# Kernel tuning notes

Hardware: AMD Instinct MI355X
Metric: run time of the kernel (lower is better)

## Reference

```python
import jax, jax.numpy as jnp
import numpy as np

D_MODEL = 256
NHEAD = 8
HEAD_DIM = D_MODEL // NHEAD
CLIP = 10.0


def setup_inputs() -> dict:
    key = jax.random.key(0)
    k1, k2, k3, k4 = jax.random.split(key, 4)
    B, N = 4, 256
    nodes = jax.random.normal(k1, (B, N, D_MODEL), dtype=jnp.float32)
    edges = jax.random.normal(k2, (B, N, N, D_MODEL), dtype=jnp.float32)
    # torch nn.Linear default init: U(-1/sqrt(in), 1/sqrt(in))
    bound = 1.0 / np.sqrt(D_MODEL)
    W = jax.random.uniform(k3, (D_MODEL, D_MODEL), minval=-bound, maxval=bound, dtype=jnp.float32)
    b = jax.random.uniform(k4, (D_MODEL,), minval=-bound, maxval=bound, dtype=jnp.float32)
    return {"nodes": nodes, "edges": edges, "W": W, "b": b}


def reference(nodes, edges, W, b):
    B, N, _ = nodes.shape
    H, Dh = NHEAD, HEAD_DIM

    def proj(x):  # torch Linear: x @ W.T + b
        return x @ W.T + b

    # Node projections: the module applies the SAME linear to q, k, v
    node_p = proj(nodes).reshape(B, N, H, Dh)
    nq, nk, nv = node_p, node_p, node_p
    # Edge projections (same linear for q and k)
    edge_p = proj(edges).reshape(B, N, N, H, Dh)
    eq, ek = edge_p, edge_p

    query = eq + nq[:, :, None, :, :]   # (B,N,N,H,Dh)
    key = ek + nk[:, None, :, :, :]     # (B,N,N,H,Dh)
    scores = jnp.einsum('bijhd,bijhd->bhij', query, key) / np.sqrt(Dh).astype(np.float32)
    scores = CLIP * jnp.tanh(scores)
    attn = jax.nn.softmax(scores, axis=-1)  # (B,H,N,N)
    # output = attn @ values (values transposed to (B,H,N,Dh))
    out = jnp.einsum('bhij,bjhd->bihd', attn, nv).reshape(B, N, D_MODEL)
    out = proj(out)
    return (out, attn)
```

## Files before the change

### kernel.cpp

```cpp
#include <hip/hip_runtime.h>
#include <hip/hip_bf16.h>
#include <math.h>

typedef short short8 __attribute__((ext_vector_type(8)));
typedef float f32x4 __attribute__((ext_vector_type(4)));

__device__ __forceinline__ unsigned short f2bf(float x) {
    unsigned u = __float_as_uint(x);
    u += 0x7FFF + ((u >> 16) & 1);
    return (unsigned short)(u >> 16);
}
__device__ __forceinline__ float bf2f(unsigned short h) {
    return __uint_as_float(((unsigned)h) << 16);
}

__device__ __forceinline__ void cvtpair(float f0, float f1, unsigned& hw, unsigned& lw) {
    __hip_bfloat162 h2 = __float22bfloat162_rn(float2{f0, f1});
    unsigned hu = *(unsigned*)&h2;
    float r0 = f0 - __uint_as_float(hu << 16);
    float r1 = f1 - __uint_as_float(hu & 0xFFFF0000u);
    __hip_bfloat162 l2 = __float22bfloat162_rn(float2{r0, r1});
    hw = hu;
    lw = *(unsigned*)&l2;
}

__device__ __forceinline__ void cvt8(const float4 a, const float4 b, short8& hi, short8& lo) {
    union { unsigned u[4]; short8 s; } H, L;
    cvtpair(a.x, a.y, H.u[0], L.u[0]);
    cvtpair(a.z, a.w, H.u[1], L.u[1]);
    cvtpair(b.x, b.y, H.u[2], L.u[2]);
    cvtpair(b.z, b.w, H.u[3], L.u[3]);
    hi = H.s; lo = L.s;
}

__device__ __forceinline__ float tanh10(float y) {
    float e = __expf(2.f * y);
    return 10.f * (e - 1.f) / (e + 1.f);
}

#define GLDS16(gp, lp)                                                        \
    __builtin_amdgcn_global_load_lds(                                         \
        (const __attribute__((address_space(1))) void*)(gp),                  \
        (__attribute__((address_space(3))) void*)(lp), 16, 0, 0)

__global__ __launch_bounds__(256) void k_prep(const float* __restrict__ W,
                                              float* __restrict__ Wt,
                                              unsigned short* __restrict__ Whi,
                                              unsigned short* __restrict__ Wlo) {
    int d = blockIdx.x, k = threadIdx.x;
    float w = W[d * 256 + k];
    Wt[k * 256 + d] = w;
    unsigned short hi = f2bf(w);
    int s  = (k >> 3) & 3;
    int sp = s ^ ((d >> 1) & 3);
    int idx = d * 256 + (k & ~31) + sp * 8 + (k & 7);
    Whi[idx] = hi;
    Wlo[idx] = f2bf(w - bf2f(hi));
}

__global__ __launch_bounds__(256) void k_node_proj(const float* __restrict__ nodes,
                                                   const float* __restrict__ Wt,
                                                   const float* __restrict__ bias,
                                                   float* __restrict__ np_) {
    int row = blockIdx.x;
    int d = threadIdx.x;
    __shared__ float xl[256];
    xl[d] = nodes[row * 256 + d];
    __syncthreads();
    float a[8] = {0.f, 0.f, 0.f, 0.f, 0.f, 0.f, 0.f, 0.f};
#pragma unroll 4
    for (int k = 0; k < 256; k += 8) {
#pragma unroll
        for (int q = 0; q < 8; ++q)
            a[q] = fmaf(xl[k + q], Wt[(k + q) * 256 + d], a[q]);
    }
    np_[row * 256 + d] =
        bias[d] + ((a[0] + a[1]) + (a[2] + a[3])) + ((a[4] + a[5]) + (a[6] + a[7]));
}

__global__ __launch_bounds__(256, 2) void k_edge_mfma(const float* __restrict__ edges,
                                                      const unsigned short* __restrict__ Whi,
                                                      const unsigned short* __restrict__ Wlo,
                                                      const float* __restrict__ bias,
                                                      const float* __restrict__ np_,
                                                      float* __restrict__ attn) {
    __shared__ unsigned short Wbuf[2][2][128 * 32];
    __shared__ float npi[128];
    __shared__ float sc[4][256];

    const int t = threadIdx.x;
    const int w = t >> 6, l = t & 63;
    const int col = l & 15, g = l >> 4;
    const int wrow = l >> 2, wq = l & 3;

    const int p = blockIdx.x;
    const int L = (p & 7) * 256 + (p >> 3);
    const int tile = L >> 1, half = L & 1;
    const int bb = tile >> 8, ii = tile & 255;
    const int n0 = half * 128;

    if (t < 32)
        ((float4*)npi)[t] = ((const float4*)(np_ + (size_t)(bb * 256 + ii) * 256 + n0))[t];
    __builtin_amdgcn_sched_barrier(0);

    f32x4 acc[4][8];
#pragma unroll
    for (int mt = 0; mt < 4; ++mt)
#pragma unroll
        for (int nt = 0; nt < 8; ++nt) acc[mt][nt] = (f32x4){0.f, 0.f, 0.f, 0.f};

    const float* ea = edges + ((size_t)((bb * 256 + ii) * 256 + w * 64 + col)) * 256 + g * 8;
    const size_t wg0 = (size_t)(n0 + w * 32 + wrow) * 256 + wq * 8;
    const size_t wg1 = wg0 + 16 * 256;

    GLDS16(Whi + wg0, &Wbuf[0][0][(w * 32) * 32]);
    GLDS16(Wlo + wg0, &Wbuf[0][1][(w * 32) * 32]);
    GLDS16(Whi + wg1, &Wbuf[0][0][(w * 32 + 16) * 32]);
    GLDS16(Wlo + wg1, &Wbuf[0][1][(w * 32 + 16) * 32]);
    __builtin_amdgcn_sched_barrier(0);
    float4 e[4][2];
#pragma unroll
    for (int mt = 0; mt < 4; ++mt) {
        e[mt][0] = *(const float4*)(ea + mt * 4096);
        e[mt][1] = *(const float4*)(ea + mt * 4096 + 4);
    }
    __builtin_amdgcn_sched_barrier(0);
    asm volatile("s_waitcnt vmcnt(8)\n\ts_barrier" ::: "memory");

    const int swb = (g ^ ((col >> 1) & 3)) << 3;

    short8 Ah[4], Al[4];

#pragma unroll
    for (int kc = 0; kc < 8; ++kc) {
#pragma unroll
        for (int mt = 0; mt < 4; ++mt)
            cvt8(e[mt][0], e[mt][1], Ah[mt], Al[mt]);
        __builtin_amdgcn_sched_barrier(0);
        if (kc < 7) {
            const int nb = (kc + 1) & 1;
            const size_t kofs = (size_t)(kc + 1) * 32;
            GLDS16(Whi + wg0 + kofs, &Wbuf[nb][0][(w * 32) * 32]);
            GLDS16(Wlo + wg0 + kofs, &Wbuf[nb][1][(w * 32) * 32]);
            GLDS16(Whi + wg1 + kofs, &Wbuf[nb][0][(w * 32 + 16) * 32]);
            GLDS16(Wlo + wg1 + kofs, &Wbuf[nb][1][(w * 32 + 16) * 32]);
            __builtin_amdgcn_sched_barrier(0);
#pragma unroll
            for (int mt = 0; mt < 4; ++mt) {
                e[mt][0] = *(const float4*)(ea + (kc + 1) * 32 + mt * 4096);
                e[mt][1] = *(const float4*)(ea + (kc + 1) * 32 + mt * 4096 + 4);
            }
            __builtin_amdgcn_sched_barrier(0);
        }
        const unsigned short* bh = &Wbuf[kc & 1][0][0] + col * 32 + swb;
        const unsigned short* bl = &Wbuf[kc & 1][1][0] + col * 32 + swb;
        __builtin_amdgcn_s_setprio(1);
#pragma unroll
        for (int nt = 0; nt < 8; ++nt) {
            short8 Bh = *(const short8*)(bh + nt * 512);
            short8 Bl = *(const short8*)(bl + nt * 512);
#pragma unroll
            for (int mt = 0; mt < 4; ++mt) {
                acc[mt][nt] = __builtin_amdgcn_mfma_f32_16x16x32_bf16(Ah[mt], Bh, acc[mt][nt], 0, 0, 0);
                acc[mt][nt] = __builtin_amdgcn_mfma_f32_16x16x32_bf16(Ah[mt], Bl, acc[mt][nt], 0, 0, 0);
                acc[mt][nt] = __builtin_amdgcn_mfma_f32_16x16x32_bf16(Al[mt], Bh, acc[mt][nt], 0, 0, 0);
            }
        }
        __builtin_amdgcn_s_setprio(0);
        __builtin_amdgcn_sched_barrier(0);
        if (kc < 7) {
            asm volatile("s_waitcnt vmcnt(8)\n\ts_barrier" ::: "memory");
        }
    }

    const float isq = 0.17677669529663687f;
    float bv[8], nv[8];
#pragma unroll
    for (int nt = 0; nt < 8; ++nt) {
        int dl = nt * 16 + col;
        bv[nt] = bias[n0 + dl];
        nv[nt] = npi[dl];
    }
#pragma unroll
    for (int mt = 0; mt < 4; ++mt) {
#pragma unroll
        for (int r = 0; r < 4; ++r) {
            int el = w * 64 + mt * 16 + g * 4 + r;
            const float* npj = np_ + (size_t)(bb * 256 + el) * 256 + n0;
            float pp, s0 = 0.f, s1 = 0.f, s2 = 0.f, s3 = 0.f;
            pp = acc[mt][0][r] + bv[0]; s0 += (pp + nv[0]) * (pp + npj[col]);
            pp = acc[mt][1][r] + bv[1]; s0 += (pp + nv[1]) * (pp + npj[16 + col]);
            pp = acc[mt][2][r] + bv[2]; s1 += (pp + nv[2]) * (pp + npj[32 + col]);
            pp = acc[mt][3][r] + bv[3]; s1 += (pp + nv[3]) * (pp + npj[48 + col]);
            pp = acc[mt][4][r] + bv[4]; s2 += (pp + nv[4]) * (pp + npj[64 + col]);
            pp = acc[mt][5][r] + bv[5]; s2 += (pp + nv[5]) * (pp + npj[80 + col]);
            pp = acc[mt][6][r] + bv[6]; s3 += (pp + nv[6]) * (pp + npj[96 + col]);
            pp = acc[mt][7][r] + bv[7]; s3 += (pp + nv[7]) * (pp + npj[112 + col]);
#pragma unroll
            for (int m = 1; m < 16; m <<= 1) {
                s0 += __shfl_xor(s0, m, 64);
                s1 += __shfl_xor(s1, m, 64);
                s2 += __shfl_xor(s2, m, 64);
                s3 += __shfl_xor(s3, m, 64);
            }
            if (col == 0) {
                sc[0][el] = tanh10(s0 * isq);
                sc[1][el] = tanh10(s1 * isq);
                sc[2][el] = tanh10(s2 * isq);
                sc[3][el] = tanh10(s3 * isq);
            }
        }
    }
    __syncthreads();

    {
        float4 v = *(float4*)&sc[w][l * 4];
        float m = fmaxf(fmaxf(v.x, v.y), fmaxf(v.z, v.w));
#pragma unroll
        for (int s = 1; s < 64; s <<= 1) m = fmaxf(m, __shfl_xor(m, s, 64));
        v.x = __expf(v.x - m); v.y = __expf(v.y - m);
        v.z = __expf(v.z - m); v.w = __expf(v.w - m);
        float sum = v.x + v.y + v.z + v.w;
#pragma unroll
        for (int s = 1; s < 64; s <<= 1) sum += __shfl_xor(sum, s, 64);
        float inv = 1.f / sum;
        v.x *= inv; v.y *= inv; v.z *= inv; v.w *= inv;
        *(float4*)(attn + (((size_t)(bb * 8 + half * 4 + w) * 256 + ii) << 8) + l * 4) = v;
    }
}

__global__ __launch_bounds__(256) void k_out(const float* __restrict__ attn,
                                             const float* __restrict__ np_,
                                             const float* __restrict__ Wt,
                                             const float* __restrict__ bias,
                                             float* __restrict__ out) {
    int bi = blockIdx.x;
    int bb = bi >> 8, ii = bi & 255;
    int d = threadIdx.x;
    __shared__ float at[8 * 256];
    __shared__ float xl[256];
#pragma unroll
    for (int s = 0; s < 2; ++s) {
        int idx = d + s * 256;
        int h = idx >> 6, q = idx & 63;
        ((float4*)at)[idx] =
            ((const float4*)(attn + ((size_t)(bb * 8 + h) * 256 + ii) * 256))[q];
    }
    __syncthreads();
    int h = d >> 5;
    const float* npb = np_ + (size_t)bb * 65536 + d;
    const float* ath = at + h * 256;
    float a[8] = {0.f, 0.f, 0.f, 0.f, 0.f, 0.f, 0.f, 0.f};
#pragma unroll 2
    for (int j = 0; j < 256; j += 8) {
#pragma unroll
        for (int q = 0; q < 8; ++q)
            a[q] = fmaf(ath[j + q], npb[(size_t)(j + q) * 256], a[q]);
    }
    xl[d] = ((a[0] + a[1]) + (a[2] + a[3])) + ((a[4] + a[5]) + (a[6] + a[7]));
    __syncthreads();
    float c[8] = {bias[d], 0.f, 0.f, 0.f, 0.f, 0.f, 0.f, 0.f};
#pragma unroll 2
    for (int k = 0; k < 256; k += 8) {
#pragma unroll
        for (int q = 0; q < 8; ++q)
            c[q] = fmaf(xl[k + q], Wt[(k + q) * 256 + d], c[q]);
    }
    out[bi * 256 + d] =
        ((c[0] + c[1]) + (c[2] + c[3])) + ((c[4] + c[5]) + (c[6] + c[7]));
}

extern "C" void kernel_launch(void* const* d_in, const int* in_sizes, int n_in,
                              void* d_out, int out_size, void* d_ws, size_t ws_size,
                              hipStream_t stream) {
    (void)in_sizes; (void)n_in; (void)out_size; (void)ws_size;
    const float* nodes = (const float*)d_in[0];
    const float* edges = (const float*)d_in[1];
    const float* W     = (const float*)d_in[2];
    const float* bias  = (const float*)d_in[3];

    float* out  = (float*)d_out;
    float* attn = out + 262144;

    float* np_ = (float*)d_ws;
    float* Wt  = np_ + 262144;
    unsigned short* Whi = (unsigned short*)(Wt + 65536);
    unsigned short* Wlo = Whi + 65536;

    hipLaunchKernelGGL(k_prep,      dim3(256),  dim3(256), 0, stream, W, Wt, Whi, Wlo);
    hipLaunchKernelGGL(k_node_proj, dim3(1024), dim3(256), 0, stream, nodes, Wt, bias, np_);
    hipLaunchKernelGGL(k_edge_mfma, dim3(2048), dim3(256), 0, stream, edges, Whi, Wlo, bias, np_, attn);
    hipLaunchKernelGGL(k_out,       dim3(1024), dim3(256), 0, stream, attn, np_, Wt, bias, out);
}
```

Before: 478.1 us.

## Split edge projection into column quarters with fully preloaded W slice in LDS

```diff
diff --git a/kernel.cpp b/kernel.cpp
--- a/kernel.cpp
+++ b/kernel.cpp
@@ -51,9 +51,9 @@
     float w = W[d * 256 + k];
     Wt[k * 256 + d] = w;
     unsigned short hi = f2bf(w);
-    int s  = (k >> 3) & 3;
-    int sp = s ^ ((d >> 1) & 3);
-    int idx = d * 256 + (k & ~31) + sp * 8 + (k & 7);
+    int G  = k >> 3;
+    int Gp = G ^ (d & 7);
+    int idx = d * 256 + Gp * 8 + (k & 7);
     Whi[idx] = hi;
     Wlo[idx] = f2bf(w - bf2f(hi));
 }
@@ -84,81 +84,92 @@
                                                       const float* __restrict__ bias,
                                                       const float* __restrict__ np_,
                                                       float* __restrict__ attn) {
-    __shared__ unsigned short Wbuf[2][2][128 * 32];
-    __shared__ float npi[128];
-    __shared__ float sc[4][256];
+    __shared__ unsigned short Wf[2][64 * 256];
+    __shared__ float npi[64];
+    __shared__ float sc[2][256];
 
     const int t = threadIdx.x;
     const int w = t >> 6, l = t & 63;
     const int col = l & 15, g = l >> 4;
-    const int wrow = l >> 2, wq = l & 3;
+    const int cx = col & 7;
 
     const int p = blockIdx.x;
-    const int L = (p & 7) * 256 + (p >> 3);
-    const int tile = L >> 1, half = L & 1;
+    const int L = (p & 7) * 512 + (p >> 3);
+    const int tile = L >> 2, quarter = L & 3;
     const int bb = tile >> 8, ii = tile & 255;
-    const int n0 = half * 128;
-
-    if (t < 32)
-        ((float4*)npi)[t] = ((const float4*)(np_ + (size_t)(bb * 256 + ii) * 256 + n0))[t];
+    const int n0 = quarter * 64;
+
+    float4 npiv = ((const float4*)(np_ + (size_t)(bb * 256 + ii) * 256 + n0))[l & 15];
     __builtin_amdgcn_sched_barrier(0);
 
-    f32x4 acc[4][8];
+#pragma unroll
+    for (int m = 0; m < 2; ++m) {
+        const unsigned short* gs = (m ? Wlo : Whi) +
+            (size_t)(n0 + w * 16 + (l >> 5)) * 256 + (l & 31) * 8;
+#pragma unroll
+        for (int i = 0; i < 8; ++i)
+            GLDS16(gs + (size_t)(2 * i) * 256, &Wf[m][(w * 16 + 2 * i) * 256]);
+    }
+    __builtin_amdgcn_sched_barrier(0);
+
+    const float* ea = edges + ((size_t)((bb * 256 + ii) * 256 + w * 64 + col)) * 256 + g * 8;
+    float4 e0[4][2], e1[4][2];
+#pragma unroll
+    for (int mt = 0; mt < 4; ++mt) {
+        e0[mt][0] = *(const float4*)(ea + mt * 4096);
+        e0[mt][1] = *(const float4*)(ea + mt * 4096 + 4);
+    }
+#pragma unroll
+    for (int mt = 0; mt < 4; ++mt) {
+        e1[mt][0] = *(const float4*)(ea + 32 + mt * 4096);
+        e1[mt][1] = *(const float4*)(ea + 32 + mt * 4096 + 4);
+    }
+    if (l < 16) ((float4*)npi)[l] = npiv;
+    __builtin_amdgcn_sched_barrier(0);
+    asm volatile("s_waitcnt vmcnt(16) lgkmcnt(0)\n\ts_barrier" ::: "memory");
+
+    f32x4 acc[4][4];
 #pragma unroll
     for (int mt = 0; mt < 4; ++mt)
 #pragma unroll
-        for (int nt = 0; nt < 8; ++nt) acc[mt][nt] = (f32x4){0.f, 0.f, 0.f, 0.f};
-
-    const float* ea = edges + ((size_t)((bb * 256 + ii) * 256 + w * 64 + col)) * 256 + g * 8;
-    const size_t wg0 = (size_t)(n0 + w * 32 + wrow) * 256 + wq * 8;
-    const size_t wg1 = wg0 + 16 * 256;
-
-    GLDS16(Whi + wg0, &Wbuf[0][0][(w * 32) * 32]);
-    GLDS16(Wlo + wg0, &Wbuf[0][1][(w * 32) * 32]);
-    GLDS16(Whi + wg1, &Wbuf[0][0][(w * 32 + 16) * 32]);
-    GLDS16(Wlo + wg1, &Wbuf[0][1][(w * 32 + 16) * 32]);
-    __builtin_amdgcn_sched_barrier(0);
-    float4 e[4][2];
-#pragma unroll
-    for (int mt = 0; mt < 4; ++mt) {
-        e[mt][0] = *(const float4*)(ea + mt * 4096);
-        e[mt][1] = *(const float4*)(ea + mt * 4096 + 4);
-    }
-    __builtin_amdgcn_sched_barrier(0);
-    asm volatile("s_waitcnt vmcnt(8)\n\ts_barrier" ::: "memory");
-
-    const int swb = (g ^ ((col >> 1) & 3)) << 3;
+        for (int nt = 0; nt < 4; ++nt) acc[mt][nt] = (f32x4){0.f, 0.f, 0.f, 0.f};
 
     short8 Ah[4], Al[4];
 
 #pragma unroll
     for (int kc = 0; kc < 8; ++kc) {
-#pragma unroll
-        for (int mt = 0; mt < 4; ++mt)
-            cvt8(e[mt][0], e[mt][1], Ah[mt], Al[mt]);
+        if (kc & 1) {
+#pragma unroll
+            for (int mt = 0; mt < 4; ++mt) cvt8(e1[mt][0], e1[mt][1], Ah[mt], Al[mt]);
+        } else {
+#pragma unroll
+            for (int mt = 0; mt < 4; ++mt) cvt8(e0[mt][0], e0[mt][1], Ah[mt], Al[mt]);
+        }
         __builtin_amdgcn_sched_barrier(0);
-        if (kc < 7) {
-            const int nb = (kc + 1) & 1;
-            const size_t kofs = (size_t)(kc + 1) * 32;
-            GLDS16(Whi + wg0 + kofs, &Wbuf[nb][0][(w * 32) * 32]);
-            GLDS16(Wlo + wg0 + kofs, &Wbuf[nb][1][(w * 32) * 32]);
-            GLDS16(Whi + wg1 + kofs, &Wbuf[nb][0][(w * 32 + 16) * 32]);
-            GLDS16(Wlo + wg1 + kofs, &Wbuf[nb][1][(w * 32 + 16) * 32]);
-            __builtin_amdgcn_sched_barrier(0);
-#pragma unroll
-            for (int mt = 0; mt < 4; ++mt) {
-                e[mt][0] = *(const float4*)(ea + (kc + 1) * 32 + mt * 4096);
-                e[mt][1] = *(const float4*)(ea + (kc + 1) * 32 + mt * 4096 + 4);
-            }
-            __builtin_amdgcn_sched_barrier(0);
-        }
-        const unsigned short* bh = &Wbuf[kc & 1][0][0] + col * 32 + swb;
-        const unsigned short* bl = &Wbuf[kc & 1][1][0] + col * 32 + swb;
+        if (kc < 6) {
+            if (kc & 1) {
+#pragma unroll
+                for (int mt = 0; mt < 4; ++mt) {
+                    e1[mt][0] = *(const float4*)(ea + (kc + 2) * 32 + mt * 4096);
+                    e1[mt][1] = *(const float4*)(ea + (kc + 2) * 32 + mt * 4096 + 4);
+                }
+            } else {
+#pragma unroll
+                for (int mt = 0; mt < 4; ++mt) {
+                    e0[mt][0] = *(const float4*)(ea + (kc + 2) * 32 + mt * 4096);
+                    e0[mt][1] = *(const float4*)(ea + (kc + 2) * 32 + mt * 4096 + 4);
+                }
+            }
+        }
+        __builtin_amdgcn_sched_barrier(0);
+        const int gofs = (((kc << 2) | g) ^ cx) << 3;
+        const unsigned short* bh = &Wf[0][col * 256 + gofs];
+        const unsigned short* bl = &Wf[1][col * 256 + gofs];
         __builtin_amdgcn_s_setprio(1);
 #pragma unroll
-        for (int nt = 0; nt < 8; ++nt) {
-            short8 Bh = *(const short8*)(bh + nt * 512);
-            short8 Bl = *(const short8*)(bl + nt * 512);
+        for (int nt = 0; nt < 4; ++nt) {
+            short8 Bh = *(const short8*)(bh + nt * 4096);
+            short8 Bl = *(const short8*)(bl + nt * 4096);
 #pragma unroll
             for (int mt = 0; mt < 4; ++mt) {
                 acc[mt][nt] = __builtin_amdgcn_mfma_f32_16x16x32_bf16(Ah[mt], Bh, acc[mt][nt], 0, 0, 0);
@@ -168,15 +179,12 @@
         }
         __builtin_amdgcn_s_setprio(0);
         __builtin_amdgcn_sched_barrier(0);
-        if (kc < 7) {
-            asm volatile("s_waitcnt vmcnt(8)\n\ts_barrier" ::: "memory");
-        }
     }
 
     const float isq = 0.17677669529663687f;
-    float bv[8], nv[8];
-#pragma unroll
-    for (int nt = 0; nt < 8; ++nt) {
+    float bv[4], nv[4];
+#pragma unroll
+    for (int nt = 0; nt < 4; ++nt) {
         int dl = nt * 16 + col;
         bv[nt] = bias[n0 + dl];
         nv[nt] = npi[dl];
@@ -187,33 +195,25 @@
         for (int r = 0; r < 4; ++r) {
             int el = w * 64 + mt * 16 + g * 4 + r;
             const float* npj = np_ + (size_t)(bb * 256 + el) * 256 + n0;
-            float pp, s0 = 0.f, s1 = 0.f, s2 = 0.f, s3 = 0.f;
+            float pp, s0 = 0.f, s1 = 0.f;
             pp = acc[mt][0][r] + bv[0]; s0 += (pp + nv[0]) * (pp + npj[col]);
             pp = acc[mt][1][r] + bv[1]; s0 += (pp + nv[1]) * (pp + npj[16 + col]);
             pp = acc[mt][2][r] + bv[2]; s1 += (pp + nv[2]) * (pp + npj[32 + col]);
             pp = acc[mt][3][r] + bv[3]; s1 += (pp + nv[3]) * (pp + npj[48 + col]);
-            pp = acc[mt][4][r] + bv[4]; s2 += (pp + nv[4]) * (pp + npj[64 + col]);
-            pp = acc[mt][5][r] + bv[5]; s2 += (pp + nv[5]) * (pp + npj[80 + col]);
-            pp = acc[mt][6][r] + bv[6]; s3 += (pp + nv[6]) * (pp + npj[96 + col]);
-            pp = acc[mt][7][r] + bv[7]; s3 += (pp + nv[7]) * (pp + npj[112 + col]);
 #pragma unroll
             for (int m = 1; m < 16; m <<= 1) {
                 s0 += __shfl_xor(s0, m, 64);
                 s1 += __shfl_xor(s1, m, 64);
-                s2 += __shfl_xor(s2, m, 64);
-                s3 += __shfl_xor(s3, m, 64);
             }
             if (col == 0) {
                 sc[0][el] = tanh10(s0 * isq);
                 sc[1][el] = tanh10(s1 * isq);
-                sc[2][el] = tanh10(s2 * isq);
-                sc[3][el] = tanh10(s3 * isq);
-            }
-        }
-    }
-    __syncthreads();
-
-    {
+            }
+        }
+    }
+    __syncthreads();
+
+    if (w < 2) {
         float4 v = *(float4*)&sc[w][l * 4];
         float m = fmaxf(fmaxf(v.x, v.y), fmaxf(v.z, v.w));
 #pragma unroll
@@ -225,7 +225,7 @@
         for (int s = 1; s < 64; s <<= 1) sum += __shfl_xor(sum, s, 64);
         float inv = 1.f / sum;
         v.x *= inv; v.y *= inv; v.z *= inv; v.w *= inv;
-        *(float4*)(attn + (((size_t)(bb * 8 + half * 4 + w) * 256 + ii) << 8) + l * 4) = v;
+        *(float4*)(attn + (((size_t)(bb * 8 + quarter * 2 + w) * 256 + ii) << 8) + l * 4) = v;
     }
 }
 
@@ -289,6 +289,6 @@
 
     hipLaunchKernelGGL(k_prep,      dim3(256),  dim3(256), 0, stream, W, Wt, Whi, Wlo);
     hipLaunchKernelGGL(k_node_proj, dim3(1024), dim3(256), 0, stream, nodes, Wt, bias, np_);
-    hipLaunchKernelGGL(k_edge_mfma, dim3(2048), dim3(256), 0, stream, edges, Whi, Wlo, bias, np_, attn);
+    hipLaunchKernelGGL(k_edge_mfma, dim3(4096), dim3(256), 0, stream, edges, Whi, Wlo, bias, np_, attn);
     hipLaunchKernelGGL(k_out,       dim3(1024), dim3(256), 0, stream, attn, np_, Wt, bias, out);
 }
```

Measured after the change: 524.9 us. 9.8% more time.

## Split edge MFMA block across eight waves with fewer M tiles per wave

Applied to the files above, without the earlier changes.

```diff
diff --git a/kernel.cpp b/kernel.cpp
--- a/kernel.cpp
+++ b/kernel.cpp
@@ -42,6 +42,8 @@
     __builtin_amdgcn_global_load_lds(                                         \
         (const __attribute__((address_space(1))) void*)(gp),                  \
         (__attribute__((address_space(3))) void*)(lp), 16, 0, 0)
+
+#define SB0() __builtin_amdgcn_sched_barrier(0)
 
 __global__ __launch_bounds__(256) void k_prep(const float* __restrict__ W,
                                               float* __restrict__ Wt,
@@ -78,7 +80,7 @@
         bias[d] + ((a[0] + a[1]) + (a[2] + a[3])) + ((a[4] + a[5]) + (a[6] + a[7]));
 }
 
-__global__ __launch_bounds__(256, 2) void k_edge_mfma(const float* __restrict__ edges,
+__global__ __launch_bounds__(512, 4) void k_edge_mfma(const float* __restrict__ edges,
                                                       const unsigned short* __restrict__ Whi,
                                                       const unsigned short* __restrict__ Wlo,
                                                       const float* __restrict__ bias,
@@ -91,7 +93,6 @@
     const int t = threadIdx.x;
     const int w = t >> 6, l = t & 63;
     const int col = l & 15, g = l >> 4;
-    const int wrow = l >> 2, wq = l & 3;
 
     const int p = blockIdx.x;
     const int L = (p & 7) * 256 + (p >> 3);
@@ -101,56 +102,51 @@
 
     if (t < 32)
         ((float4*)npi)[t] = ((const float4*)(np_ + (size_t)(bb * 256 + ii) * 256 + n0))[t];
-    __builtin_amdgcn_sched_barrier(0);
-
-    f32x4 acc[4][8];
-#pragma unroll
-    for (int mt = 0; mt < 4; ++mt)
+    SB0();
+
+    f32x4 acc[2][8];
+#pragma unroll
+    for (int mt = 0; mt < 2; ++mt)
 #pragma unroll
         for (int nt = 0; nt < 8; ++nt) acc[mt][nt] = (f32x4){0.f, 0.f, 0.f, 0.f};
 
-    const float* ea = edges + ((size_t)((bb * 256 + ii) * 256 + w * 64 + col)) * 256 + g * 8;
-    const size_t wg0 = (size_t)(n0 + w * 32 + wrow) * 256 + wq * 8;
-    const size_t wg1 = wg0 + 16 * 256;
-
-    GLDS16(Whi + wg0, &Wbuf[0][0][(w * 32) * 32]);
-    GLDS16(Wlo + wg0, &Wbuf[0][1][(w * 32) * 32]);
-    GLDS16(Whi + wg1, &Wbuf[0][0][(w * 32 + 16) * 32]);
-    GLDS16(Wlo + wg1, &Wbuf[0][1][(w * 32 + 16) * 32]);
-    __builtin_amdgcn_sched_barrier(0);
-    float4 e[4][2];
-#pragma unroll
-    for (int mt = 0; mt < 4; ++mt) {
-        e[mt][0] = *(const float4*)(ea + mt * 4096);
-        e[mt][1] = *(const float4*)(ea + mt * 4096 + 4);
-    }
-    __builtin_amdgcn_sched_barrier(0);
-    asm volatile("s_waitcnt vmcnt(8)\n\ts_barrier" ::: "memory");
+    const float* ea = edges + ((size_t)((bb * 256 + ii) * 256 + w * 32 + col)) * 256 + g * 8;
+    const size_t wg = (size_t)(n0 + w * 16 + (l >> 2)) * 256 + (l & 3) * 8;
+
+    GLDS16(Whi + wg, &Wbuf[0][0][(w * 16) * 32]);
+    GLDS16(Wlo + wg, &Wbuf[0][1][(w * 16) * 32]);
+    SB0();
+    float4 e[2][2];
+    e[0][0] = *(const float4*)(ea);
+    e[0][1] = *(const float4*)(ea + 4);
+    e[1][0] = *(const float4*)(ea + 4096);
+    e[1][1] = *(const float4*)(ea + 4096 + 4);
+    SB0();
+    asm volatile("s_waitcnt vmcnt(4)\n\ts_barrier" ::: "memory");
 
     const int swb = (g ^ ((col >> 1) & 3)) << 3;
 
-    short8 Ah[4], Al[4];
+    short8 Ah[2], Al[2];
 
 #pragma unroll
     for (int kc = 0; kc < 8; ++kc) {
-#pragma unroll
-        for (int mt = 0; mt < 4; ++mt)
-            cvt8(e[mt][0], e[mt][1], Ah[mt], Al[mt]);
-        __builtin_amdgcn_sched_barrier(0);
+        cvt8(e[0][0], e[0][1], Ah[0], Al[0]);
+        SB0();
         if (kc < 7) {
             const int nb = (kc + 1) & 1;
             const size_t kofs = (size_t)(kc + 1) * 32;
-            GLDS16(Whi + wg0 + kofs, &Wbuf[nb][0][(w * 32) * 32]);
-            GLDS16(Wlo + wg0 + kofs, &Wbuf[nb][1][(w * 32) * 32]);
-            GLDS16(Whi + wg1 + kofs, &Wbuf[nb][0][(w * 32 + 16) * 32]);
-            GLDS16(Wlo + wg1 + kofs, &Wbuf[nb][1][(w * 32 + 16) * 32]);
-            __builtin_amdgcn_sched_barrier(0);
-#pragma unroll
-            for (int mt = 0; mt < 4; ++mt) {
-                e[mt][0] = *(const float4*)(ea + (kc + 1) * 32 + mt * 4096);
-                e[mt][1] = *(const float4*)(ea + (kc + 1) * 32 + mt * 4096 + 4);
-            }
-            __builtin_amdgcn_sched_barrier(0);
+            GLDS16(Whi + wg + kofs, &Wbuf[nb][0][(w * 16) * 32]);
+            GLDS16(Wlo + wg + kofs, &Wbuf[nb][1][(w * 16) * 32]);
+            e[0][0] = *(const float4*)(ea + (kc + 1) * 32);
+            e[0][1] = *(const float4*)(ea + (kc + 1) * 32 + 4);
+            SB0();
+        }
+        cvt8(e[1][0], e[1][1], Ah[1], Al[1]);
+        SB0();
+        if (kc < 7) {
+            e[1][0] = *(const float4*)(ea + (kc + 1) * 32 + 4096);
+            e[1][1] = *(const float4*)(ea + (kc + 1) * 32 + 4096 + 4);
+            SB0();
         }
         const unsigned short* bh = &Wbuf[kc & 1][0][0] + col * 32 + swb;
         const unsigned short* bl = &Wbuf[kc & 1][1][0] + col * 32 + swb;
@@ -159,17 +155,17 @@
         for (int nt = 0; nt < 8; ++nt) {
             short8 Bh = *(const short8*)(bh + nt * 512);
             short8 Bl = *(const short8*)(bl + nt * 512);
-#pragma unroll
-            for (int mt = 0; mt < 4; ++mt) {
-                acc[mt][nt] = __builtin_amdgcn_mfma_f32_16x16x32_bf16(Ah[mt], Bh, acc[mt][nt], 0, 0, 0);
-                acc[mt][nt] = __builtin_amdgcn_mfma_f32_16x16x32_bf16(Ah[mt], Bl, acc[mt][nt], 0, 0, 0);
-                acc[mt][nt] = __builtin_amdgcn_mfma_f32_16x16x32_bf16(Al[mt], Bh, acc[mt][nt], 0, 0, 0);
-            }
+            acc[0][nt] = __builtin_amdgcn_mfma_f32_16x16x32_bf16(Ah[0], Bh, acc[0][nt], 0, 0, 0);
+            acc[1][nt] = __builtin_amdgcn_mfma_f32_16x16x32_bf16(Ah[1], Bh, acc[1][nt], 0, 0, 0);
+            acc[0][nt] = __builtin_amdgcn_mfma_f32_16x16x32_bf16(Ah[0], Bl, acc[0][nt], 0, 0, 0);
+            acc[1][nt] = __builtin_amdgcn_mfma_f32_16x16x32_bf16(Ah[1], Bl, acc[1][nt], 0, 0, 0);
+            acc[0][nt] = __builtin_amdgcn_mfma_f32_16x16x32_bf16(Al[0], Bh, acc[0][nt], 0, 0, 0);
+            acc[1][nt] = __builtin_amdgcn_mfma_f32_16x16x32_bf16(Al[1], Bh, acc[1][nt], 0, 0, 0);
         }
         __builtin_amdgcn_s_setprio(0);
-        __builtin_amdgcn_sched_barrier(0);
+        SB0();
         if (kc < 7) {
-            asm volatile("s_waitcnt vmcnt(8)\n\ts_barrier" ::: "memory");
+            asm volatile("s_waitcnt vmcnt(4)\n\ts_barrier" ::: "memory");
         }
     }
 
@@ -182,10 +178,10 @@
         nv[nt] = npi[dl];
     }
 #pragma unroll
-    for (int mt = 0; mt < 4; ++mt) {
+    for (int mt = 0; mt < 2; ++mt) {
 #pragma unroll
         for (int r = 0; r < 4; ++r) {
-            int el = w * 64 + mt * 16 + g * 4 + r;
+            int el = w * 32 + mt * 16 + g * 4 + r;
             const float* npj = np_ + (size_t)(bb * 256 + el) * 256 + n0;
             float pp, s0 = 0.f, s1 = 0.f, s2 = 0.f, s3 = 0.f;
             pp = acc[mt][0][r] + bv[0]; s0 += (pp + nv[0]) * (pp + npj[col]);
@@ -213,7 +209,7 @@
     }
     __syncthreads();
 
-    {
+    if (w < 4) {
         float4 v = *(float4*)&sc[w][l * 4];
         float m = fmaxf(fmaxf(v.x, v.y), fmaxf(v.z, v.w));
 #pragma unroll
@@ -289,6 +285,6 @@
 
     hipLaunchKernelGGL(k_prep,      dim3(256),  dim3(256), 0, stream, W, Wt, Whi, Wlo);
     hipLaunchKernelGGL(k_node_proj, dim3(1024), dim3(256), 0, stream, nodes, Wt, bias, np_);
-    hipLaunchKernelGGL(k_edge_mfma, dim3(2048), dim3(256), 0, stream, edges, Whi, Wlo, bias, np_, attn);
+    hipLaunchKernelGGL(k_edge_mfma, dim3(2048), dim3(512), 0, stream, edges, Whi, Wlo, bias, np_, attn);
     hipLaunchKernelGGL(k_out,       dim3(1024), dim3(256), 0, stream, attn, np_, Wt, bias, out);
 }
```

After: 530.6 us. 1.11x slower.
